# Kernel tuning notes

Hardware: AMD Instinct MI355X
Metric: run time of the kernel (lower is better)

Reference implementation:

```python
import jax, jax.numpy as jnp
import numpy as np

B, T, C, H = 1, 2048, 1024, 16
K = C // H


def _ln(x, g, b):
    m = x.mean(-1, keepdims=True)
    v = ((x - m) ** 2).mean(-1, keepdims=True)
    return (x - m) * jax.lax.rsqrt(v + 1e-5) * g + b


def setup_inputs() -> dict:
    key = jax.random.key(0)
    ks = jax.random.split(key, 16)
    n = lambda k, s, sc=1.0: jax.random.normal(k, s, jnp.float32) * sc
    u = lambda k, s: jax.random.uniform(k, s, jnp.float32)
    ws = C ** -0.5
    return {
        "x": n(ks[0], (B, T, C)),
        "shift_state": n(ks[1], (B, C)),
        "time_maa_x": u(ks[2], (1, 1, C)),
        "time_maa_r": u(ks[3], (1, 1, C)),
        "time_maa_k": u(ks[4], (1, 1, C)),
        "time_maa_v": u(ks[5], (1, 1, C)),
        "time_maa_w1": n(ks[6], (C, 96), 0.01),
        "time_maa_w2": n(ks[7], (3, 32, C), 0.01),
        "headavg_w1": n(ks[8], (C, 4 * 2 * H), 0.01),
        "headavg_w2": n(ks[9], (4, 2 * H, H), 0.01),
        "w_r": n(ks[10], (C, C), ws),
        "w_k": n(ks[11], (C, C), ws),
        "w_v": n(ks[12], (C, C), ws),
        "w_o": n(ks[13], (C, C), ws),
        "ln_r_g": jnp.ones((C,)), "ln_r_b": jnp.zeros((C,)),
        "ln_k_g": jnp.ones((C,)), "ln_k_b": jnp.zeros((C,)),
        "ln_v_g": jnp.ones((C,)), "ln_v_b": jnp.zeros((C,)),
        "ln_x_g": jnp.ones((C,)), "ln_x_b": jnp.zeros((C,)),
    }


def reference(x, shift_state, time_maa_x, time_maa_r, time_maa_k, time_maa_v,
              time_maa_w1, time_maa_w2, headavg_w1, headavg_w2,
              w_r, w_k, w_v, w_o,
              ln_r_g, ln_r_b, ln_k_g, ln_k_b, ln_v_g, ln_v_b, ln_x_g, ln_x_b):
    Bs, Ts, Cs = x.shape
    Hh = headavg_w2.shape[-1]
    Kk = Cs // Hh

    # token shift
    dxprev = jnp.concatenate([shift_state[:, None, :], x[:, :-1]], axis=1) - x

    # LoRA token-shift mixing
    xxx = jnp.tanh((x + dxprev * time_maa_x) @ time_maa_w1)       # [B,T,3*32]
    mix = jnp.einsum('btnd,ndc->nbtc', xxx.reshape(Bs, Ts, 3, -1), time_maa_w2)
    mq, mk, mv = mix[0], mix[1], mix[2]
    xq = x + dxprev * (time_maa_r + mq)
    xk = x + dxprev * (time_maa_k + mk)
    xv = x + dxprev * (time_maa_v + mv)

    q = _ln(xq @ w_r, ln_r_g, ln_r_b).reshape(Bs, Ts, Hh, Kk).transpose(0, 2, 1, 3)
    k = _ln(xk @ w_k, ln_k_g, ln_k_b).reshape(Bs, Ts, Hh, Kk).transpose(0, 2, 1, 3)
    v = _ln(xv @ w_v, ln_v_g, ln_v_b).reshape(Bs, Ts, Hh, Kk).transpose(0, 2, 1, 3)

    # per-head LoRA score mixing coefficients
    ha = jnp.tanh(x @ headavg_w1).reshape(Bs, Ts, 4, -1)          # [B,T,4,2H]
    hm = jnp.einsum('btnd,ndh->nbth', ha, headavg_w2) / Hh        # [4,B,T,H]
    pre_q, pre_k, post_q, post_k = hm[0], hm[1], hm[2], hm[3]

    scale = Kk ** -0.5
    y = jnp.einsum('bhtk,bhsk->bhts', q * scale, k)               # [B,H,T,S]
    y = y + jnp.einsum('bhts,bth->bts', y, pre_q)[:, None]
    y = y + jnp.einsum('bhts,bsh->bts', y, pre_k)[:, None]

    # causal ALiBi bias
    rel = (jnp.arange(Ts)[:, None] - jnp.arange(Ts)[None, :]).astype(x.dtype)
    slopes = (2.0 ** (-8.0 * jnp.arange(1, Hh + 1, dtype=x.dtype) / Hh))
    bias = jnp.where(rel >= 0, -slopes[:, None, None] * rel, jnp.asarray(-1e9, x.dtype))
    y = y + bias[None]

    y = jax.nn.softmax(y, axis=-1)
    y = y + jnp.einsum('bhts,bth->bts', y, post_q)[:, None]
    y = y + jnp.einsum('bhts,bsh->bts', y, post_k)[:, None]

    out = jnp.einsum('bhts,bhsv->bhtv', y, v).transpose(0, 2, 1, 3).reshape(Bs, Ts, Cs)
    out = _ln(out, ln_x_g, ln_x_b) @ w_o
    return out
```

## Files before the change

### kernel.cpp

```cpp
#include <hip/hip_runtime.h>
#include <cstdint>
#include <cstddef>


#define C_DIM 1024
#define HEADS 16
#define TQ 16
#define SCH 256
#define PADS 40
#define EPS 36

typedef unsigned short ushort_t;
typedef __attribute__((ext_vector_type(8))) short bf16x8;
typedef __attribute__((ext_vector_type(4))) float f32x4;

#define MFMA16(a, b, c) __builtin_amdgcn_mfma_f32_16x16x32_bf16(a, b, c, 0, 0, 0)

__device__ __forceinline__ unsigned int f2bf_u(float f) {
  unsigned int u = __float_as_uint(f);
  return (u + 0x7fffu + ((u >> 16) & 1u)) >> 16;
}
__device__ __forceinline__ float bf2f(ushort_t u) {
  return __uint_as_float(((unsigned int)u) << 16);
}
__device__ __forceinline__ void pack4(ushort_t* dst, float x0, float x1,
                                      float x2, float x3) {
  uint2 v;
  v.x = f2bf_u(x0) | (f2bf_u(x1) << 16);
  v.y = f2bf_u(x2) | (f2bf_u(x3) << 16);
  *(uint2*)dst = v;
}
__device__ __forceinline__ void mlmerge(float& M, float& L, float m2, float l2) {
  float nm = fmaxf(M, m2);
  float ea = (M  <= -1e29f) ? 0.f : __expf(M - nm);
  float eb = (m2 <= -1e29f) ? 0.f : __expf(m2 - nm);
  L = L * ea + l2 * eb;
  M = nm;
}

__global__ __launch_bounds__(256) void prep_kernel(
    const float* __restrict__ x, const float* __restrict__ shift,
    const float* __restrict__ maa_x,
    float* __restrict__ dxprev, ushort_t* __restrict__ zbf,
    ushort_t* __restrict__ xbf)
{
  const int t = blockIdx.x;
  const int c = threadIdx.x * 4;
  const size_t base = (size_t)t * C_DIM + c;
  const float4 xc = *(const float4*)&x[base];
  const float4 xp = (t == 0) ? *(const float4*)&shift[c]
                             : *(const float4*)&x[base - C_DIM];
  const float4 mx = *(const float4*)&maa_x[c];
  float4 d;
  d.x = xp.x - xc.x; d.y = xp.y - xc.y; d.z = xp.z - xc.z; d.w = xp.w - xc.w;
  *(float4*)&dxprev[base] = d;
  pack4(&zbf[base], xc.x + d.x*mx.x, xc.y + d.y*mx.y,
        xc.z + d.z*mx.z, xc.w + d.w*mx.w);
  pack4(&xbf[base], xc.x, xc.y, xc.z, xc.w);
}

__global__ __launch_bounds__(256) void wlora_prep(
    const float* __restrict__ w1, const float* __restrict__ hw1,
    ushort_t* __restrict__ wlt)
{
  __shared__ float tile[32][33];
  const int k0 = blockIdx.x*32, j0 = blockIdx.y*32;
  const int r = threadIdx.x >> 3, c4 = (threadIdx.x & 7) * 4;
  const float* W = (j0 < 96) ? w1 : hw1;
  const int stride = (j0 < 96) ? 96 : 128;
  const int jo = (j0 < 96) ? j0 : j0 - 96;
  const float4 v = *(const float4*)&W[(size_t)(k0+r)*stride + jo + c4];
  tile[r][c4+0] = v.x; tile[r][c4+1] = v.y;
  tile[r][c4+2] = v.z; tile[r][c4+3] = v.w;
  __syncthreads();
  pack4(&wlt[(size_t)(j0+r)*C_DIM + k0 + c4],
        tile[c4+0][r], tile[c4+1][r], tile[c4+2][r], tile[c4+3][r]);
}

__global__ __launch_bounds__(64) void lora_gemm(
    const ushort_t* __restrict__ zbf, const ushort_t* __restrict__ xbf,
    const ushort_t* __restrict__ wlt, float* __restrict__ xxx,
    float* __restrict__ ha)
{
  const int nt = blockIdx.y;
  const int bm = blockIdx.x * 32;
  const ushort_t* A = (nt < 3) ? zbf : xbf;
  const int wrow = nt * 32;
  const int lane = threadIdx.x;
  const int l15 = lane & 15, g = lane >> 4;
  f32x4 acc[2][2];
  #pragma unroll
  for (int i = 0; i < 2; i++)
    #pragma unroll
    for (int j = 0; j < 2; j++) acc[i][j] = (f32x4){0.f,0.f,0.f,0.f};
  bf16x8 a0[2], b0[2], a1[2], b1[2];
  #define LLA(dst, kk) { \
    dst[0] = *(const bf16x8*)&A[(size_t)(bm + l15)*C_DIM + (kk) + g*8]; \
    dst[1] = *(const bf16x8*)&A[(size_t)(bm + 16 + l15)*C_DIM + (kk) + g*8]; }
  #define LLB(dst, kk) { \
    dst[0] = *(const bf16x8*)&wlt[(size_t)(wrow + l15)*C_DIM + (kk) + g*8]; \
    dst[1] = *(const bf16x8*)&wlt[(size_t)(wrow + 16 + l15)*C_DIM + (kk) + g*8]; }
  LLA(a0, 0); LLB(b0, 0);
  for (int k0 = 0; k0 < C_DIM; k0 += 64) {
    LLA(a1, k0+32); LLB(b1, k0+32);
    #pragma unroll
    for (int i = 0; i < 2; i++)
      #pragma unroll
      for (int j = 0; j < 2; j++) acc[i][j] = MFMA16(a0[i], b0[j], acc[i][j]);
    if (k0 + 64 < C_DIM) { LLA(a0, k0+64); LLB(b0, k0+64); }
    #pragma unroll
    for (int i = 0; i < 2; i++)
      #pragma unroll
      for (int j = 0; j < 2; j++) acc[i][j] = MFMA16(a1[i], b1[j], acc[i][j]);
  }
  #undef LLA
  #undef LLB
  #pragma unroll
  for (int i = 0; i < 2; i++)
    #pragma unroll
    for (int j = 0; j < 2; j++)
      #pragma unroll
      for (int r = 0; r < 4; r++) {
        const int t = bm + i*16 + g*4 + r;
        const int col = wrow + j*16 + l15;
        const float val = tanhf(acc[i][j][r]);
        if (nt < 3) xxx[(size_t)t*96 + col] = val;
        else        ha[(size_t)t*128 + col - 96] = val;
      }
}

__global__ __launch_bounds__(256) void mix_kernel(
    const float* __restrict__ x, const float* __restrict__ dxp,
    const float* __restrict__ xxx,
    const float* __restrict__ maa_r, const float* __restrict__ maa_k,
    const float* __restrict__ maa_v, const float* __restrict__ w2,
    ushort_t* __restrict__ xq, ushort_t* __restrict__ xk,
    ushort_t* __restrict__ xv)
{
  __shared__ float xs[8][96];
  const int t0 = blockIdx.x * 8;
  const int tid = threadIdx.x;
  #pragma unroll
  for (int i = 0; i < 3; i++) {
    const int u = tid + i*256;
    if (u < 768) {
      const int r = u / 96, cc = u % 96;
      xs[r][cc] = xxx[(size_t)(t0+r)*96 + cc];
    }
  }
  __syncthreads();
  const int c = tid * 4;
  float4 xc[8], dx[8];
  #pragma unroll
  for (int r = 0; r < 8; r++) {
    xc[r] = *(const float4*)&x[(size_t)(t0+r)*C_DIM + c];
    dx[r] = *(const float4*)&dxp[(size_t)(t0+r)*C_DIM + c];
  }
  const float* maas[3] = {maa_r, maa_k, maa_v};
  ushort_t* outs[3] = {xq, xk, xv};
  #pragma unroll
  for (int n = 0; n < 3; n++) {
    const float4 mv = *(const float4*)&maas[n][c];
    float m[8][4];
    #pragma unroll
    for (int r = 0; r < 8; r++) {
      m[r][0] = mv.x; m[r][1] = mv.y; m[r][2] = mv.z; m[r][3] = mv.w;
    }
    #pragma unroll 8
    for (int d = 0; d < 32; d++) {
      const float4 w = *(const float4*)&w2[((size_t)n*32 + d)*C_DIM + c];
      #pragma unroll
      for (int r = 0; r < 8; r++) {
        const float xv2 = xs[r][n*32 + d];
        m[r][0] += xv2*w.x; m[r][1] += xv2*w.y;
        m[r][2] += xv2*w.z; m[r][3] += xv2*w.w;
      }
    }
    #pragma unroll
    for (int r = 0; r < 8; r++)
      pack4(&outs[n][(size_t)(t0+r)*C_DIM + c],
            xc[r].x + dx[r].x*m[r][0], xc[r].y + dx[r].y*m[r][1],
            xc[r].z + dx[r].z*m[r][2], xc[r].w + dx[r].w*m[r][3]);
  }
}

__global__ __launch_bounds__(256) void hm_kernel(
    const float* __restrict__ ha, const float* __restrict__ hw2,
    float* __restrict__ hm, int T)
{
  const int t = blockIdx.x*4 + (threadIdx.x >> 6);
  const int u = threadIdx.x & 63;
  const int n = u >> 4, h = u & 15;
  float s = 0.f;
  #pragma unroll 8
  for (int d = 0; d < 32; d++)
    s += ha[(size_t)t*128 + n*32 + d] * hw2[(size_t)(n*32 + d)*16 + h];
  hm[((size_t)n*T + t)*16 + h] = s * (1.f/16.f);
}

__global__ __launch_bounds__(256) void wprep_kernel(
    const float* __restrict__ w0, const float* __restrict__ w1,
    const float* __restrict__ w2, const float* __restrict__ w3,
    ushort_t* __restrict__ o0, ushort_t* __restrict__ o1,
    ushort_t* __restrict__ o2, ushort_t* __restrict__ o3)
{
  const float* W; ushort_t* O;
  if (blockIdx.z == 0)      { W = w0; O = o0; }
  else if (blockIdx.z == 1) { W = w1; O = o1; }
  else if (blockIdx.z == 2) { W = w2; O = o2; }
  else                      { W = w3; O = o3; }
  __shared__ float tile[32][33];
  const int k0 = blockIdx.x*32, n0 = blockIdx.y*32;
  const int r = threadIdx.x >> 3, c4 = (threadIdx.x & 7) * 4;
  const float4 v = *(const float4*)&W[(size_t)(k0+r)*C_DIM + n0 + c4];
  tile[r][c4+0] = v.x; tile[r][c4+1] = v.y;
  tile[r][c4+2] = v.z; tile[r][c4+3] = v.w;
  __syncthreads();
  pack4(&O[(size_t)(n0+r)*C_DIM + k0 + c4],
        tile[c4+0][r], tile[c4+1][r], tile[c4+2][r], tile[c4+3][r]);
}

__global__ __launch_bounds__(64) void gemm_bf16(
    const ushort_t* __restrict__ A, const ushort_t* __restrict__ Bt,
    float* __restrict__ Cm)
{
  const int bid = blockIdx.x;
  const int bn = (bid & 15) * 64;
  const int bm = (bid >> 4) * 32;
  const int lane = threadIdx.x;
  const int l15 = lane & 15, g = lane >> 4;
  f32x4 acc[2][4];
  #pragma unroll
  for (int i = 0; i < 2; i++)
    #pragma unroll
    for (int j = 0; j < 4; j++) acc[i][j] = (f32x4){0.f,0.f,0.f,0.f};
  bf16x8 a0[2], b0[4], a1[2], b1[4];
  #define LGA(dst, kk) { \
    _Pragma("unroll") \
    for (int i = 0; i < 2; i++) \
      dst[i] = *(const bf16x8*)&A[(size_t)(bm + i*16 + l15)*C_DIM + (kk) + g*8]; }
  #define LGB(dst, kk) { \
    _Pragma("unroll") \
    for (int j = 0; j < 4; j++) \
      dst[j] = *(const bf16x8*)&Bt[(size_t)(bn + j*16 + l15)*C_DIM + (kk) + g*8]; }
  LGA(a0, 0); LGB(b0, 0);
  for (int k0 = 0; k0 < C_DIM; k0 += 64) {
    LGA(a1, k0+32); LGB(b1, k0+32);
    #pragma unroll
    for (int i = 0; i < 2; i++)
      #pragma unroll
      for (int j = 0; j < 4; j++) acc[i][j] = MFMA16(a0[i], b0[j], acc[i][j]);
    if (k0 + 64 < C_DIM) { LGA(a0, k0+64); LGB(b0, k0+64); }
    #pragma unroll
    for (int i = 0; i < 2; i++)
      #pragma unroll
      for (int j = 0; j < 4; j++) acc[i][j] = MFMA16(a1[i], b1[j], acc[i][j]);
  }
  #undef LGA
  #undef LGB
  #pragma unroll
  for (int i = 0; i < 2; i++)
    #pragma unroll
    for (int j = 0; j < 4; j++)
      #pragma unroll
      for (int r = 0; r < 4; r++)
        Cm[(size_t)(bm + i*16 + g*4 + r)*C_DIM + bn + j*16 + l15] = acc[i][j][r];
}

__global__ __launch_bounds__(256) void ln_rows(
    const float* __restrict__ in, ushort_t* __restrict__ outp,
    const float* __restrict__ g, const float* __restrict__ b, float scale)
{
  __shared__ float red[4];
  const int t = blockIdx.x;
  const int tid = threadIdx.x;
  const int c = tid*4;
  const float4 v = *(const float4*)&in[(size_t)t*C_DIM + c];
  float s = v.x+v.y+v.z+v.w;
  #pragma unroll
  for (int off = 32; off > 0; off >>= 1) s += __shfl_down(s, off, 64);
  if ((tid & 63) == 0) red[tid >> 6] = s;
  __syncthreads();
  const float mean = (red[0]+red[1]+red[2]+red[3]) * (1.0f/C_DIM);
  __syncthreads();
  const float d0 = v.x-mean, d1 = v.y-mean, d2 = v.z-mean, d3 = v.w-mean;
  float q = d0*d0 + d1*d1 + d2*d2 + d3*d3;
  #pragma unroll
  for (int off = 32; off > 0; off >>= 1) q += __shfl_down(q, off, 64);
  if ((tid & 63) == 0) red[tid >> 6] = q;
  __syncthreads();
  const float var = (red[0]+red[1]+red[2]+red[3]) * (1.0f/C_DIM);
  const float rstd = rsqrtf(var + 1e-5f);
  const float4 gv = *(const float4*)&g[c];
  const float4 bv = *(const float4*)&b[c];
  pack4(outp + (size_t)t*C_DIM + c,
        (d0*rstd*gv.x + bv.x)*scale, (d1*rstd*gv.y + bv.y)*scale,
        (d2*rstd*gv.z + bv.z)*scale, (d3*rstd*gv.w + bv.w)*scale);
}

__global__ __launch_bounds__(256) void vtrans_kernel(
    const ushort_t* __restrict__ vbf, ushort_t* __restrict__ Vt, int T)
{
  __shared__ ushort_t tile[32][36];
  const int t0 = blockIdx.x*32, c0 = blockIdx.y*32;
  const int r = threadIdx.x >> 3, c4 = (threadIdx.x & 7) * 4;
  const uint2 raw = *(const uint2*)&vbf[(size_t)(t0+r)*C_DIM + c0 + c4];
  tile[r][c4+0] = (ushort_t)(raw.x & 0xffffu);
  tile[r][c4+1] = (ushort_t)(raw.x >> 16);
  tile[r][c4+2] = (ushort_t)(raw.y & 0xffffu);
  tile[r][c4+3] = (ushort_t)(raw.y >> 16);
  __syncthreads();
  uint2 w;
  w.x = (unsigned)tile[c4+0][r] | ((unsigned)tile[c4+1][r] << 16);
  w.y = (unsigned)tile[c4+2][r] | ((unsigned)tile[c4+3][r] << 16);
  *(uint2*)&Vt[(size_t)(c0+r)*T + t0 + c4] = w;
}

__global__ __launch_bounds__(256) void qek_prep(
    const ushort_t* __restrict__ qbf, const ushort_t* __restrict__ kbf,
    const float* __restrict__ hmb, ushort_t* __restrict__ Qe,
    ushort_t* __restrict__ Ke, float* __restrict__ spo_g, int T)
{
  const int t = blockIdx.x;
  const int tid = threadIdx.x;
  const int c4 = tid * 4;
  const int h = tid >> 4;
  float sp = 0.f, so = 0.f;
  #pragma unroll
  for (int q4 = 0; q4 < 4; q4++) {
    const float4 v = *(const float4*)&hmb[((size_t)1*T + t)*16 + q4*4];
    sp += v.x + v.y + v.z + v.w;
    const float4 o = *(const float4*)&hmb[((size_t)3*T + t)*16 + q4*4];
    so += o.x + o.y + o.z + o.w;
  }
  if (tid == 0) spo_g[t] = so;
  const float preq = hmb[((size_t)0*T + t)*16 + h];
  const float prek = hmb[((size_t)1*T + t)*16 + h];
  const uint2 qr = *(const uint2*)&qbf[(size_t)t*C_DIM + c4];
  const uint2 kr = *(const uint2*)&kbf[(size_t)t*C_DIM + c4];
  float qv[4], kv[4];
  qv[0] = bf2f((ushort_t)(qr.x & 0xffffu)); qv[1] = bf2f((ushort_t)(qr.x >> 16));
  qv[2] = bf2f((ushort_t)(qr.y & 0xffffu)); qv[3] = bf2f((ushort_t)(qr.y >> 16));
  kv[0] = bf2f((ushort_t)(kr.x & 0xffffu)); kv[1] = bf2f((ushort_t)(kr.x >> 16));
  kv[2] = bf2f((ushort_t)(kr.y & 0xffffu)); kv[3] = bf2f((ushort_t)(kr.y >> 16));
  const size_t rb = (size_t)t * 2048;
  pack4(&Qe[rb + c4], qv[0]*preq, qv[1]*preq, qv[2]*preq, qv[3]*preq);
  *(uint2*)&Qe[rb + 1024 + c4] = qr;
  const float osp = 1.f + sp;
  pack4(&Ke[rb + c4], kv[0]*osp, kv[1]*osp, kv[2]*osp, kv[3]*osp);
  pack4(&Ke[rb + 1024 + c4], kv[0]*prek, kv[1]*prek, kv[2]*prek, kv[3]*prek);
}

__global__ __launch_bounds__(64) void e_gemm(
    const ushort_t* __restrict__ Qe, const ushort_t* __restrict__ Ke,
    float* __restrict__ E, int T)
{
  const int bm = blockIdx.y * 32;
  const int bn = blockIdx.x * 64;
  if (bn > bm + 31) return;
  const int lane = threadIdx.x;
  const int l15 = lane & 15, g = lane >> 4;
  const int KD = 2048;
  f32x4 acc[2][4];
  #pragma unroll
  for (int i = 0; i < 2; i++)
    #pragma unroll
    for (int j = 0; j < 4; j++) acc[i][j] = (f32x4){0.f,0.f,0.f,0.f};
  bf16x8 a0[2], b0[4], a1[2], b1[4];
  #define LEA(dst, kk) { \
    _Pragma("unroll") \
    for (int i = 0; i < 2; i++) \
      dst[i] = *(const bf16x8*)&Qe[(size_t)(bm + i*16 + l15)*KD + (kk) + g*8]; }
  #define LEB(dst, kk) { \
    _Pragma("unroll") \
    for (int j = 0; j < 4; j++) \
      dst[j] = *(const bf16x8*)&Ke[(size_t)(bn + j*16 + l15)*KD + (kk) + g*8]; }
  LEA(a0, 0); LEB(b0, 0);
  for (int k0 = 0; k0 < KD; k0 += 64) {
    LEA(a1, k0+32); LEB(b1, k0+32);
    #pragma unroll
    for (int i = 0; i < 2; i++)
      #pragma unroll
      for (int j = 0; j < 4; j++) acc[i][j] = MFMA16(a0[i], b0[j], acc[i][j]);
    if (k0 + 64 < KD) { LEA(a0, k0+64); LEB(b0, k0+64); }
    #pragma unroll
    for (int i = 0; i < 2; i++)
      #pragma unroll
      for (int j = 0; j < 4; j++) acc[i][j] = MFMA16(a1[i], b1[j], acc[i][j]);
  }
  #undef LEA
  #undef LEB
  #pragma unroll
  for (int i = 0; i < 2; i++)
    #pragma unroll
    for (int j = 0; j < 4; j++)
      #pragma unroll
      for (int r = 0; r < 4; r++)
        E[(size_t)(bm + i*16 + g*4 + r)*T + bn + j*16 + l15] = acc[i][j][r];
}

__global__ __launch_bounds__(512) void attn_stats(
    const ushort_t* __restrict__ qbf, const ushort_t* __restrict__ kbf,
    const float* __restrict__ E, float* __restrict__ part_m,
    float* __restrict__ part_l, int T)
{
  const int tbi = (int)blockIdx.y;
  const int tb = (T/TQ) - 1 - tbi;
  const int sc = (tbi & 1) ? (7 - (int)blockIdx.x) : (int)blockIdx.x;
  const int t0 = tb * TQ;
  const int sbeg = sc * SCH;
  if (sbeg >= t0 + TQ) return;
  const int send = (sbeg + SCH < t0 + TQ) ? (sbeg + SCH) : (t0 + TQ);

  const int tid = threadIdx.x;
  const int w = tid >> 6, lane = tid & 63, l15 = lane & 15, g = lane >> 4;
  const int hh[2] = {w, w + 8};
  bf16x8 qf[2][2];
  float slope[2];
  #pragma unroll
  for (int hd = 0; hd < 2; hd++) {
    #pragma unroll
    for (int kc = 0; kc < 2; kc++)
      qf[hd][kc] = *(const bf16x8*)
          &qbf[(size_t)(t0 + l15)*C_DIM + hh[hd]*64 + kc*32 + g*8];
    slope[hd] = exp2f(-0.5f * (float)(hh[hd] + 1));
  }
  float mrun[2] = {-1e30f, -1e30f}, lrun[2] = {0.f, 0.f};

  bf16x8 kf[2][2][2];
  float4 ef[2];
  #define LOADK(sbase) { \
    _Pragma("unroll") \
    for (int hd = 0; hd < 2; hd++) \
      _Pragma("unroll") \
      for (int sh = 0; sh < 2; sh++) \
        _Pragma("unroll") \
        for (int kc = 0; kc < 2; kc++) \
          kf[hd][sh][kc] = *(const bf16x8*)&kbf[ \
              (size_t)((sbase) + sh*16 + l15)*C_DIM + hh[hd]*64 + kc*32 + g*8]; }
  #define LOADE(sbase) { \
    _Pragma("unroll") \
    for (int sh = 0; sh < 2; sh++) \
      ef[sh] = *(const float4*)&E[(size_t)(t0 + l15)*T + (sbase) + sh*16 + g*4]; }
  LOADK(sbeg); LOADE(sbeg);

  for (int s1 = sbeg; s1 < send; s1 += 32) {
    f32x4 acc[2][2];
    #pragma unroll
    for (int hd = 0; hd < 2; hd++)
      #pragma unroll
      for (int sh = 0; sh < 2; sh++) acc[hd][sh] = (f32x4){0.f,0.f,0.f,0.f};
    #pragma unroll
    for (int hd = 0; hd < 2; hd++)
      #pragma unroll
      for (int sh = 0; sh < 2; sh++)
        #pragma unroll
        for (int kc = 0; kc < 2; kc++)
          acc[hd][sh] = MFMA16(kf[hd][sh][kc], qf[hd][kc], acc[hd][sh]);
    float efc[2][4];
    #pragma unroll
    for (int sh = 0; sh < 2; sh++) *(float4*)efc[sh] = ef[sh];
    {
      const int snx = (s1 + 32 < send) ? s1 + 32 : s1;
      LOADK(snx); LOADE(snx);
    }
    #pragma unroll
    for (int hd = 0; hd < 2; hd++) {
      const int t = t0 + l15;
      #pragma unroll
      for (int sh = 0; sh < 2; sh++)
        #pragma unroll
        for (int r = 0; r < 4; r++) {
          const int s = s1 + sh*16 + g*4 + r;
          if (s <= t) {
            const float y3 = acc[hd][sh][r] + efc[sh][r]
                - slope[hd]*(float)(t - s);
            const float d = y3 - mrun[hd];
            if (d > 0.f) { lrun[hd] = lrun[hd]*__expf(-d) + 1.f; mrun[hd] = y3; }
            else lrun[hd] += __expf(d);
          }
        }
    }
  }
  #undef LOADK
  #undef LOADE
  #pragma unroll
  for (int hd = 0; hd < 2; hd++) {
    float M = mrun[hd], L = lrun[hd];
    #pragma unroll
    for (int mask = 16; mask < 64; mask <<= 1) {
      const float M2 = __shfl_xor(M, mask, 64);
      const float L2 = __shfl_xor(L, mask, 64);
      mlmerge(M, L, M2, L2);
    }
    if (g == 0) {
      part_m[(size_t)(sc*HEADS + hh[hd])*T + t0 + l15] = M;
      part_l[(size_t)(sc*HEADS + hh[hd])*T + t0 + l15] = L;
    }
  }
}

__global__ __launch_bounds__(256) void ml_combine(
    const float* __restrict__ part_m, const float* __restrict__ part_l,
    float* __restrict__ m_fin, float* __restrict__ linv, int T)
{
  const int idx = blockIdx.x*256 + threadIdx.x;
  const int t = idx & (T - 1);
  const int nsc = (t >> 8) + 1;
  float M = -1e30f, L = 0.f;
  for (int sc = 0; sc < nsc; sc++)
    mlmerge(M, L, part_m[(size_t)sc*HEADS*T + idx],
            part_l[(size_t)sc*HEADS*T + idx]);
  m_fin[idx] = M;
  linv[idx] = 1.f / L;
}

__global__ __launch_bounds__(512) void attn_apply(
    const ushort_t* __restrict__ qbf, const ushort_t* __restrict__ kbf,
    const ushort_t* __restrict__ Vt, const float* __restrict__ E,
    const float* __restrict__ hmb, const float* __restrict__ spo_g,
    const float* __restrict__ m_fin, const float* __restrict__ linv,
    float* __restrict__ P, int T)
{
  __shared__ ushort_t ybuf[HEADS*TQ*PADS];
  __shared__ float ep[TQ*EPS];

  const int tbi = (int)blockIdx.y;
  const int tb = (T/TQ) - 1 - tbi;
  const int sc = (tbi & 1) ? (7 - (int)blockIdx.x) : (int)blockIdx.x;
  const int t0 = tb * TQ;
  const int sbeg = sc * SCH;
  if (sbeg >= t0 + TQ) return;
  const int send = (sbeg + SCH < t0 + TQ) ? (sbeg + SCH) : (t0 + TQ);
  const int prow0 = T*sc - 128*sc*(sc-1) - SCH*sc;

  const int tid = threadIdx.x;
  const int w = tid >> 6, lane = tid & 63, l15 = lane & 15, g = lane >> 4;

  const int hh[2] = {w, w + 8};
  bf16x8 qf[2][2];
  float mt[2], li[2], slope[2];
  #pragma unroll
  for (int hd = 0; hd < 2; hd++) {
    #pragma unroll
    for (int kc = 0; kc < 2; kc++)
      qf[hd][kc] = *(const bf16x8*)
          &qbf[(size_t)(t0 + l15)*C_DIM + hh[hd]*64 + kc*32 + g*8];
    mt[hd] = m_fin[(size_t)hh[hd]*T + t0 + l15];
    li[hd] = linv[(size_t)hh[hd]*T + t0 + l15];
    slope[hd] = exp2f(-0.5f * (float)(hh[hd] + 1));
  }
  f32x4 oacc[2][4];
  #pragma unroll
  for (int hd = 0; hd < 2; hd++)
    #pragma unroll
    for (int vf = 0; vf < 4; vf++) oacc[hd][vf] = (f32x4){0.f,0.f,0.f,0.f};

  for (int s1 = sbeg; s1 < send; s1 += 32) {
    f32x4 acc[2][2];
    #pragma unroll
    for (int hd = 0; hd < 2; hd++)
      #pragma unroll
      for (int sh = 0; sh < 2; sh++) acc[hd][sh] = (f32x4){0.f,0.f,0.f,0.f};
    float4 ef[2];
    #pragma unroll
    for (int sh = 0; sh < 2; sh++)
      ef[sh] = *(const float4*)&E[(size_t)(t0 + l15)*T + s1 + sh*16 + g*4];
    #pragma unroll
    for (int hd = 0; hd < 2; hd++)
      #pragma unroll
      for (int sh = 0; sh < 2; sh++)
        #pragma unroll
        for (int kc = 0; kc < 2; kc++) {
          const bf16x8 kf = *(const bf16x8*)
              &kbf[(size_t)(s1 + sh*16 + l15)*C_DIM + hh[hd]*64 + kc*32 + g*8];
          acc[hd][sh] = MFMA16(kf, qf[hd][kc], acc[hd][sh]);
        }
    #pragma unroll
    for (int hd = 0; hd < 2; hd++) {
      const int t = t0 + l15;
      #pragma unroll
      for (int sh = 0; sh < 2; sh++) {
        #pragma unroll
        for (int r = 0; r < 4; r++) {
          const int s = s1 + sh*16 + g*4 + r;
          float p = 0.f;
          if (s <= t) {
            const float y3 = acc[hd][sh][r] + ef[sh][r]
                - slope[hd]*(float)(t - s);
            p = __expf(y3 - mt[hd]) * li[hd];
          }
          acc[hd][sh][r] = p;
        }
        pack4(&ybuf[(size_t)(hh[hd]*TQ + l15)*PADS + sh*16 + g*4],
              acc[hd][sh][0], acc[hd][sh][1], acc[hd][sh][2], acc[hd][sh][3]);
      }
    }
    __syncthreads();
    if (tid < 128) {
      const int tcq = tid >> 3, sq = tid & 7;
      const int s0g = s1 + sq*4;
      const float* hoqr = &hmb[((size_t)2*T + t0 + tcq)*16];
      float a4[4] = {0.f,0.f,0.f,0.f}, b4[4] = {0.f,0.f,0.f,0.f};
      #pragma unroll
      for (int hq4 = 0; hq4 < 4; hq4++) {
        float hqa[4];
        *(float4*)hqa = *(const float4*)&hoqr[hq4*4];
        float hka[4][4];
        #pragma unroll
        for (int c = 0; c < 4; c++)
          *(float4*)hka[c] =
              *(const float4*)&hmb[((size_t)3*T + s0g + c)*16 + hq4*4];
        #pragma unroll
        for (int j = 0; j < 4; j++) {
          const uint2 yr = *(const uint2*)
              &ybuf[((hq4*4 + j)*TQ + tcq)*PADS + sq*4];
          float yv[4];
          yv[0] = bf2f((ushort_t)(yr.x & 0xffffu));
          yv[1] = bf2f((ushort_t)(yr.x >> 16));
          yv[2] = bf2f((ushort_t)(yr.y & 0xffffu));
          yv[3] = bf2f((ushort_t)(yr.y >> 16));
          #pragma unroll
          for (int c = 0; c < 4; c++) {
            a4[c] += yv[c] * hqa[j];
            b4[c] += yv[c] * hka[c][j];
          }
        }
      }
      float ssum[4];
      *(float4*)ssum = *(const float4*)&spo_g[s0g];
      float4 eo;
      eo.x = a4[0]*(1.f + ssum[0]) + b4[0];
      eo.y = a4[1]*(1.f + ssum[1]) + b4[1];
      eo.z = a4[2]*(1.f + ssum[2]) + b4[2];
      eo.w = a4[3]*(1.f + ssum[3]) + b4[3];
      *(float4*)&ep[tcq*EPS + sq*4] = eo;
    }
    __syncthreads();
    bf16x8 vv[2][4];
    #pragma unroll
    for (int hd = 0; hd < 2; hd++)
      #pragma unroll
      for (int vf = 0; vf < 4; vf++)
        vv[hd][vf] = *(const bf16x8*)
            &Vt[(size_t)(hh[hd]*64 + vf*16 + l15)*T + s1 + g*8];
    {
      float epv[2][4];
      #pragma unroll
      for (int sh = 0; sh < 2; sh++)
        *(float4*)epv[sh] = *(const float4*)&ep[l15*EPS + sh*16 + g*4];
      #pragma unroll
      for (int hd = 0; hd < 2; hd++)
        #pragma unroll
        for (int sh = 0; sh < 2; sh++)
          pack4(&ybuf[(size_t)(hh[hd]*TQ + l15)*PADS + sh*16 + g*4],
                acc[hd][sh][0] + epv[sh][0], acc[hd][sh][1] + epv[sh][1],
                acc[hd][sh][2] + epv[sh][2], acc[hd][sh][3] + epv[sh][3]);
    }
    #pragma unroll
    for (int hd = 0; hd < 2; hd++) {
      const bf16x8 pa = *(const bf16x8*)
          &ybuf[(size_t)(hh[hd]*TQ + l15)*PADS + g*8];
      #pragma unroll
      for (int vf = 0; vf < 4; vf++)
        oacc[hd][vf] = MFMA16(pa, vv[hd][vf], oacc[hd][vf]);
    }
  }
  #pragma unroll
  for (int hd = 0; hd < 2; hd++)
    #pragma unroll
    for (int vf = 0; vf < 4; vf++)
      #pragma unroll
      for (int r = 0; r < 4; r++)
        P[(size_t)(prow0 + t0 + g*4 + r)*C_DIM + hh[hd]*64 + vf*16 + l15]
            = oacc[hd][vf][r];
}

__global__ __launch_bounds__(256) void reduce_ln(
    const float* __restrict__ P, ushort_t* __restrict__ outp,
    const float* __restrict__ g, const float* __restrict__ b, int T)
{
  __shared__ float red[4];
  const int t = blockIdx.x;
  const int tid = threadIdx.x;
  const int c = tid*4;
  const int nsc = (t >> 8) + 1;
  float4 v = make_float4(0.f, 0.f, 0.f, 0.f);
  int off = 0;
  for (int sc = 0; sc < nsc; sc++) {
    const int row = off + t - sc*SCH;
    const float4 pv = *(const float4*)&P[(size_t)row*C_DIM + c];
    v.x += pv.x; v.y += pv.y; v.z += pv.z; v.w += pv.w;
    off += T - SCH*sc;
  }
  float s = v.x+v.y+v.z+v.w;
  #pragma unroll
  for (int o = 32; o > 0; o >>= 1) s += __shfl_down(s, o, 64);
  if ((tid & 63) == 0) red[tid >> 6] = s;
  __syncthreads();
  const float mean = (red[0]+red[1]+red[2]+red[3]) * (1.0f/C_DIM);
  __syncthreads();
  const float d0 = v.x-mean, d1 = v.y-mean, d2 = v.z-mean, d3 = v.w-mean;
  float q = d0*d0 + d1*d1 + d2*d2 + d3*d3;
  #pragma unroll
  for (int o = 32; o > 0; o >>= 1) q += __shfl_down(q, o, 64);
  if ((tid & 63) == 0) red[tid >> 6] = q;
  __syncthreads();
  const float var = (red[0]+red[1]+red[2]+red[3]) * (1.0f/C_DIM);
  const float rstd = rsqrtf(var + 1e-5f);
  const float4 gv = *(const float4*)&g[c];
  const float4 bv = *(const float4*)&b[c];
  pack4(outp + (size_t)t*C_DIM + c,
        d0*rstd*gv.x + bv.x, d1*rstd*gv.y + bv.y,
        d2*rstd*gv.z + bv.z, d3*rstd*gv.w + bv.w);
}

extern "C" void kernel_launch(void* const* d_in, const int* in_sizes, int n_in,
                              void* d_out, int out_size, void* d_ws, size_t ws_size,
                              hipStream_t stream)
{
  const float* x      = (const float*)d_in[0];
  const float* shift  = (const float*)d_in[1];
  const float* maa_x  = (const float*)d_in[2];
  const float* maa_r  = (const float*)d_in[3];
  const float* maa_k  = (const float*)d_in[4];
  const float* maa_v  = (const float*)d_in[5];
  const float* w1     = (const float*)d_in[6];
  const float* w2     = (const float*)d_in[7];
  const float* hw1    = (const float*)d_in[8];
  const float* hw2    = (const float*)d_in[9];
  const float* w_r    = (const float*)d_in[10];
  const float* w_k    = (const float*)d_in[11];
  const float* w_v    = (const float*)d_in[12];
  const float* w_o    = (const float*)d_in[13];
  const float* ln_r_g = (const float*)d_in[14];
  const float* ln_r_b = (const float*)d_in[15];
  const float* ln_k_g = (const float*)d_in[16];
  const float* ln_k_b = (const float*)d_in[17];
  const float* ln_v_g = (const float*)d_in[18];
  const float* ln_v_b = (const float*)d_in[19];
  const float* ln_x_g = (const float*)d_in[20];
  const float* ln_x_b = (const float*)d_in[21];

  const int T = in_sizes[0] / C_DIM;
  const size_t MM = (size_t)T * C_DIM;
  const size_t HF = MM / 2;

  float* ws = (float*)d_ws;
  float*    P      = ws;
  float*    dxprev = ws;
  ushort_t* zbf    = (ushort_t*)(ws + MM);
  ushort_t* xbf    = (ushort_t*)(ws + MM + HF);
  float*    gtmp   = ws + 2*MM;
  ushort_t* xqb    = (ushort_t*)(ws + 3*MM);
  ushort_t* xkb    = (ushort_t*)(ws + 3*MM + HF);
  ushort_t* xvb    = (ushort_t*)(ws + 4*MM);
  ushort_t* Qe = (ushort_t*)gtmp;
  ushort_t* Ke = (ushort_t*)(ws + 3*MM);
  float* base2 = ws + 4*MM + HF;
  ushort_t* qbf = (ushort_t*)(base2 + 0*HF);
  ushort_t* kbf = (ushort_t*)(base2 + 1*HF);
  ushort_t* vbf = (ushort_t*)(base2 + 2*HF);
  ushort_t* Vt  = (ushort_t*)(base2 + 3*HF);
  ushort_t* wtr = (ushort_t*)(base2 + 4*HF);
  ushort_t* wtk = wtr + (size_t)C_DIM*C_DIM;
  ushort_t* wtv = wtk + (size_t)C_DIM*C_DIM;
  ushort_t* wto = wtv + (size_t)C_DIM*C_DIM;
  float* after_w = base2 + 4*HF + (size_t)2*C_DIM*C_DIM;
  ushort_t* wlt = (ushort_t*)after_w;
  float* xxx    = after_w + 131072;
  float* ha     = xxx + (size_t)T*96;
  float* hmb    = ha + (size_t)T*128;
  float* part_m = hmb + (size_t)4*T*16;
  float* part_l = part_m + (size_t)8*HEADS*T;
  float* m_fin  = part_l + (size_t)8*HEADS*T;
  float* linv   = m_fin + (size_t)HEADS*T;
  float* spo_g  = linv + (size_t)HEADS*T;
  float* abf_f  = spo_g + (size_t)T;
  ushort_t* abf = (ushort_t*)abf_f;
  float* Ebuf   = abf_f + HF;

  prep_kernel<<<T, 256, 0, stream>>>(x, shift, maa_x, dxprev, zbf, xbf);
  wlora_prep<<<dim3(C_DIM/32, 7), 256, 0, stream>>>(w1, hw1, wlt);
  lora_gemm<<<dim3(T/32, 7), 64, 0, stream>>>(zbf, xbf, wlt, xxx, ha);
  mix_kernel<<<T/8, 256, 0, stream>>>(x, dxprev, xxx, maa_r, maa_k, maa_v, w2,
                                      xqb, xkb, xvb);
  hm_kernel<<<T/4, 256, 0, stream>>>(ha, hw2, hmb, T);
  wprep_kernel<<<dim3(32, 32, 4), 256, 0, stream>>>(
      w_r, w_k, w_v, w_o, wtr, wtk, wtv, wto);

  const int ggemm = (T/32) * (C_DIM/64);
  gemm_bf16<<<ggemm, 64, 0, stream>>>(xqb, wtr, gtmp);
  ln_rows<<<T, 256, 0, stream>>>(gtmp, qbf, ln_r_g, ln_r_b, 0.125f);
  gemm_bf16<<<ggemm, 64, 0, stream>>>(xkb, wtk, gtmp);
  ln_rows<<<T, 256, 0, stream>>>(gtmp, kbf, ln_k_g, ln_k_b, 1.0f);
  gemm_bf16<<<ggemm, 64, 0, stream>>>(xvb, wtv, gtmp);
  ln_rows<<<T, 256, 0, stream>>>(gtmp, vbf, ln_v_g, ln_v_b, 1.0f);
  vtrans_kernel<<<dim3(T/32, C_DIM/32), 256, 0, stream>>>(vbf, Vt, T);

  qek_prep<<<T, 256, 0, stream>>>(qbf, kbf, hmb, Qe, Ke, spo_g, T);
  e_gemm<<<dim3(T/64, T/32), 64, 0, stream>>>(Qe, Ke, Ebuf, T);

  attn_stats<<<dim3(8, T/TQ), 512, 0, stream>>>(
      qbf, kbf, Ebuf, part_m, part_l, T);
  ml_combine<<<(HEADS*T)/256, 256, 0, stream>>>(part_m, part_l, m_fin, linv, T);
  attn_apply<<<dim3(8, T/TQ), 512, 0, stream>>>(
      qbf, kbf, Vt, Ebuf, hmb, spo_g, m_fin, linv, P, T);

  reduce_ln<<<T, 256, 0, stream>>>(P, abf, ln_x_g, ln_x_b, T);
  gemm_bf16<<<ggemm, 64, 0, stream>>>(abf, wto, (float*)d_out);
}
```

Measured before the change: 576.9 us.

## Cache pre-softmax scores in fp16 between attention passes and shrink GEMM tiles

attn_stats now writes the computed pre-softmax score (QK plus E term plus ALiBi) to a compact fp16 buffer indexed by a triangular offset. attn_apply reads those scores back instead of reloading q/k and redoing the QK MFMAs and E reads. Separately, the projection GEMMs and e_gemm move from 32x64 to 32x32 tiles, which doubles the number of blocks and gives finer causal skipping in e_gemm. The costs are extra global traffic for the score buffer, fp16 rounding of the scores, and less operand reuse per block in the GEMMs.

```diff
diff --git a/kernel.cpp b/kernel.cpp
--- a/kernel.cpp
+++ b/kernel.cpp
@@ -1,4 +1,5 @@
 #include <hip/hip_runtime.h>
+#include <hip/hip_fp16.h>
 #include <cstdint>
 #include <cstddef>
 
@@ -36,6 +37,11 @@
   float eb = (m2 <= -1e29f) ? 0.f : __expf(m2 - nm);
   L = L * ea + l2 * eb;
   M = nm;
+}
+__device__ __forceinline__ int y3_off(int tbi) {
+  const int m = tbi >> 1;
+  const int S = m*(m-1) + ((tbi & 1) ? m : 0);
+  return 64*tbi - S;
 }
 
 __global__ __launch_bounds__(256) void prep_kernel(
@@ -225,23 +231,23 @@
     float* __restrict__ Cm)
 {
   const int bid = blockIdx.x;
-  const int bn = (bid & 15) * 64;
-  const int bm = (bid >> 4) * 32;
+  const int bn = (bid & 31) * 32;
+  const int bm = (bid >> 5) * 32;
   const int lane = threadIdx.x;
   const int l15 = lane & 15, g = lane >> 4;
-  f32x4 acc[2][4];
+  f32x4 acc[2][2];
   #pragma unroll
   for (int i = 0; i < 2; i++)
     #pragma unroll
-    for (int j = 0; j < 4; j++) acc[i][j] = (f32x4){0.f,0.f,0.f,0.f};
-  bf16x8 a0[2], b0[4], a1[2], b1[4];
+    for (int j = 0; j < 2; j++) acc[i][j] = (f32x4){0.f,0.f,0.f,0.f};
+  bf16x8 a0[2], b0[2], a1[2], b1[2];
   #define LGA(dst, kk) { \
     _Pragma("unroll") \
     for (int i = 0; i < 2; i++) \
       dst[i] = *(const bf16x8*)&A[(size_t)(bm + i*16 + l15)*C_DIM + (kk) + g*8]; }
   #define LGB(dst, kk) { \
     _Pragma("unroll") \
-    for (int j = 0; j < 4; j++) \
+    for (int j = 0; j < 2; j++) \
       dst[j] = *(const bf16x8*)&Bt[(size_t)(bn + j*16 + l15)*C_DIM + (kk) + g*8]; }
   LGA(a0, 0); LGB(b0, 0);
   for (int k0 = 0; k0 < C_DIM; k0 += 64) {
@@ -249,19 +255,19 @@
     #pragma unroll
     for (int i = 0; i < 2; i++)
       #pragma unroll
-      for (int j = 0; j < 4; j++) acc[i][j] = MFMA16(a0[i], b0[j], acc[i][j]);
+      for (int j = 0; j < 2; j++) acc[i][j] = MFMA16(a0[i], b0[j], acc[i][j]);
     if (k0 + 64 < C_DIM) { LGA(a0, k0+64); LGB(b0, k0+64); }
     #pragma unroll
     for (int i = 0; i < 2; i++)
       #pragma unroll
-      for (int j = 0; j < 4; j++) acc[i][j] = MFMA16(a1[i], b1[j], acc[i][j]);
+      for (int j = 0; j < 2; j++) acc[i][j] = MFMA16(a1[i], b1[j], acc[i][j]);
   }
   #undef LGA
   #undef LGB
   #pragma unroll
   for (int i = 0; i < 2; i++)
     #pragma unroll
-    for (int j = 0; j < 4; j++)
+    for (int j = 0; j < 2; j++)
       #pragma unroll
       for (int r = 0; r < 4; r++)
         Cm[(size_t)(bm + i*16 + g*4 + r)*C_DIM + bn + j*16 + l15] = acc[i][j][r];
@@ -355,25 +361,25 @@
     const ushort_t* __restrict__ Qe, const ushort_t* __restrict__ Ke,
     float* __restrict__ E, int T)
 {
+  if ((int)blockIdx.x > (int)blockIdx.y) return;
   const int bm = blockIdx.y * 32;
-  const int bn = blockIdx.x * 64;
-  if (bn > bm + 31) return;
+  const int bn = blockIdx.x * 32;
   const int lane = threadIdx.x;
   const int l15 = lane & 15, g = lane >> 4;
   const int KD = 2048;
-  f32x4 acc[2][4];
+  f32x4 acc[2][2];
   #pragma unroll
   for (int i = 0; i < 2; i++)
     #pragma unroll
-    for (int j = 0; j < 4; j++) acc[i][j] = (f32x4){0.f,0.f,0.f,0.f};
-  bf16x8 a0[2], b0[4], a1[2], b1[4];
+    for (int j = 0; j < 2; j++) acc[i][j] = (f32x4){0.f,0.f,0.f,0.f};
+  bf16x8 a0[2], b0[2], a1[2], b1[2];
   #define LEA(dst, kk) { \
     _Pragma("unroll") \
     for (int i = 0; i < 2; i++) \
       dst[i] = *(const bf16x8*)&Qe[(size_t)(bm + i*16 + l15)*KD + (kk) + g*8]; }
   #define LEB(dst, kk) { \
     _Pragma("unroll") \
-    for (int j = 0; j < 4; j++) \
+    for (int j = 0; j < 2; j++) \
       dst[j] = *(const bf16x8*)&Ke[(size_t)(bn + j*16 + l15)*KD + (kk) + g*8]; }
   LEA(a0, 0); LEB(b0, 0);
   for (int k0 = 0; k0 < KD; k0 += 64) {
@@ -381,19 +387,19 @@
     #pragma unroll
     for (int i = 0; i < 2; i++)
       #pragma unroll
-      for (int j = 0; j < 4; j++) acc[i][j] = MFMA16(a0[i], b0[j], acc[i][j]);
+      for (int j = 0; j < 2; j++) acc[i][j] = MFMA16(a0[i], b0[j], acc[i][j]);
     if (k0 + 64 < KD) { LEA(a0, k0+64); LEB(b0, k0+64); }
     #pragma unroll
     for (int i = 0; i < 2; i++)
       #pragma unroll
-      for (int j = 0; j < 4; j++) acc[i][j] = MFMA16(a1[i], b1[j], acc[i][j]);
+      for (int j = 0; j < 2; j++) acc[i][j] = MFMA16(a1[i], b1[j], acc[i][j]);
   }
   #undef LEA
   #undef LEB
   #pragma unroll
   for (int i = 0; i < 2; i++)
     #pragma unroll
-    for (int j = 0; j < 4; j++)
+    for (int j = 0; j < 2; j++)
       #pragma unroll
       for (int r = 0; r < 4; r++)
         E[(size_t)(bm + i*16 + g*4 + r)*T + bn + j*16 + l15] = acc[i][j][r];
@@ -402,7 +408,7 @@
 __global__ __launch_bounds__(512) void attn_stats(
     const ushort_t* __restrict__ qbf, const ushort_t* __restrict__ kbf,
     const float* __restrict__ E, float* __restrict__ part_m,
-    float* __restrict__ part_l, int T)
+    float* __restrict__ part_l, ushort_t* __restrict__ y3d, int T)
 {
   const int tbi = (int)blockIdx.y;
   const int tb = (T/TQ) - 1 - tbi;
@@ -411,6 +417,7 @@
   const int sbeg = sc * SCH;
   if (sbeg >= t0 + TQ) return;
   const int send = (sbeg + SCH < t0 + TQ) ? (sbeg + SCH) : (t0 + TQ);
+  const int offT = y3_off(tbi);
 
   const int tid = threadIdx.x;
   const int w = tid >> 6, lane = tid & 63, l15 = lane & 15, g = lane >> 4;
@@ -464,22 +471,30 @@
       const int snx = (s1 + 32 < send) ? s1 + 32 : s1;
       LOADK(snx); LOADE(snx);
     }
+    ushort_t* slot = y3d + ((size_t)(offT + (s1 >> 5))*512 + tid)*16;
     #pragma unroll
     for (int hd = 0; hd < 2; hd++) {
       const int t = t0 + l15;
       #pragma unroll
-      for (int sh = 0; sh < 2; sh++)
+      for (int sh = 0; sh < 2; sh++) {
+        float y3v[4];
         #pragma unroll
         for (int r = 0; r < 4; r++) {
           const int s = s1 + sh*16 + g*4 + r;
+          y3v[r] = acc[hd][sh][r] + efc[sh][r] - slope[hd]*(float)(t - s);
           if (s <= t) {
-            const float y3 = acc[hd][sh][r] + efc[sh][r]
-                - slope[hd]*(float)(t - s);
-            const float d = y3 - mrun[hd];
-            if (d > 0.f) { lrun[hd] = lrun[hd]*__expf(-d) + 1.f; mrun[hd] = y3; }
+            const float d = y3v[r] - mrun[hd];
+            if (d > 0.f) { lrun[hd] = lrun[hd]*__expf(-d) + 1.f; mrun[hd] = y3v[r]; }
             else lrun[hd] += __expf(d);
           }
         }
+        __half2 h0 = __floats2half2_rn(y3v[0], y3v[1]);
+        __half2 h1 = __floats2half2_rn(y3v[2], y3v[3]);
+        uint2 pk;
+        pk.x = *(unsigned*)&h0;
+        pk.y = *(unsigned*)&h1;
+        *(uint2*)(slot + (hd*2 + sh)*4) = pk;
+      }
     }
   }
   #undef LOADK
@@ -516,8 +531,7 @@
 }
 
 __global__ __launch_bounds__(512) void attn_apply(
-    const ushort_t* __restrict__ qbf, const ushort_t* __restrict__ kbf,
-    const ushort_t* __restrict__ Vt, const float* __restrict__ E,
+    const ushort_t* __restrict__ y3d, const ushort_t* __restrict__ Vt,
     const float* __restrict__ hmb, const float* __restrict__ spo_g,
     const float* __restrict__ m_fin, const float* __restrict__ linv,
     float* __restrict__ P, int T)
@@ -533,22 +547,16 @@
   if (sbeg >= t0 + TQ) return;
   const int send = (sbeg + SCH < t0 + TQ) ? (sbeg + SCH) : (t0 + TQ);
   const int prow0 = T*sc - 128*sc*(sc-1) - SCH*sc;
+  const int offT = y3_off(tbi);
 
   const int tid = threadIdx.x;
   const int w = tid >> 6, lane = tid & 63, l15 = lane & 15, g = lane >> 4;
-
   const int hh[2] = {w, w + 8};
-  bf16x8 qf[2][2];
-  float mt[2], li[2], slope[2];
+  float mt[2], li[2];
   #pragma unroll
   for (int hd = 0; hd < 2; hd++) {
-    #pragma unroll
-    for (int kc = 0; kc < 2; kc++)
-      qf[hd][kc] = *(const bf16x8*)
-          &qbf[(size_t)(t0 + l15)*C_DIM + hh[hd]*64 + kc*32 + g*8];
     mt[hd] = m_fin[(size_t)hh[hd]*T + t0 + l15];
     li[hd] = linv[(size_t)hh[hd]*T + t0 + l15];
-    slope[hd] = exp2f(-0.5f * (float)(hh[hd] + 1));
   }
   f32x4 oacc[2][4];
   #pragma unroll
@@ -557,39 +565,22 @@
     for (int vf = 0; vf < 4; vf++) oacc[hd][vf] = (f32x4){0.f,0.f,0.f,0.f};
 
   for (int s1 = sbeg; s1 < send; s1 += 32) {
+    const ushort_t* slot = y3d + ((size_t)(offT + (s1 >> 5))*512 + tid)*16;
     f32x4 acc[2][2];
-    #pragma unroll
-    for (int hd = 0; hd < 2; hd++)
-      #pragma unroll
-      for (int sh = 0; sh < 2; sh++) acc[hd][sh] = (f32x4){0.f,0.f,0.f,0.f};
-    float4 ef[2];
-    #pragma unroll
-    for (int sh = 0; sh < 2; sh++)
-      ef[sh] = *(const float4*)&E[(size_t)(t0 + l15)*T + s1 + sh*16 + g*4];
-    #pragma unroll
-    for (int hd = 0; hd < 2; hd++)
-      #pragma unroll
-      for (int sh = 0; sh < 2; sh++)
-        #pragma unroll
-        for (int kc = 0; kc < 2; kc++) {
-          const bf16x8 kf = *(const bf16x8*)
-              &kbf[(size_t)(s1 + sh*16 + l15)*C_DIM + hh[hd]*64 + kc*32 + g*8];
-          acc[hd][sh] = MFMA16(kf, qf[hd][kc], acc[hd][sh]);
-        }
     #pragma unroll
     for (int hd = 0; hd < 2; hd++) {
       const int t = t0 + l15;
       #pragma unroll
       for (int sh = 0; sh < 2; sh++) {
+        const uint2 pk = *(const uint2*)(slot + (hd*2 + sh)*4);
+        const float2 f0 = __half22float2(*(const __half2*)&pk.x);
+        const float2 f1 = __half22float2(*(const __half2*)&pk.y);
+        const float y3v[4] = {f0.x, f0.y, f1.x, f1.y};
         #pragma unroll
         for (int r = 0; r < 4; r++) {
           const int s = s1 + sh*16 + g*4 + r;
           float p = 0.f;
-          if (s <= t) {
-            const float y3 = acc[hd][sh][r] + ef[sh][r]
-                - slope[hd]*(float)(t - s);
-            p = __expf(y3 - mt[hd]) * li[hd];
-          }
+          if (s <= t) p = __expf(y3v[r] - mt[hd]) * li[hd];
           acc[hd][sh][r] = p;
         }
         pack4(&ybuf[(size_t)(hh[hd]*TQ + l15)*PADS + sh*16 + g*4],
@@ -779,6 +770,7 @@
   float* abf_f  = spo_g + (size_t)T;
   ushort_t* abf = (ushort_t*)abf_f;
   float* Ebuf   = abf_f + HF;
+  ushort_t* y3d = (ushort_t*)(Ebuf + (size_t)T*T);
 
   prep_kernel<<<T, 256, 0, stream>>>(x, shift, maa_x, dxprev, zbf, xbf);
   wlora_prep<<<dim3(C_DIM/32, 7), 256, 0, stream>>>(w1, hw1, wlt);
@@ -789,7 +781,7 @@
   wprep_kernel<<<dim3(32, 32, 4), 256, 0, stream>>>(
       w_r, w_k, w_v, w_o, wtr, wtk, wtv, wto);
 
-  const int ggemm = (T/32) * (C_DIM/64);
+  const int ggemm = (T/32) * (C_DIM/32);
   gemm_bf16<<<ggemm, 64, 0, stream>>>(xqb, wtr, gtmp);
   ln_rows<<<T, 256, 0, stream>>>(gtmp, qbf, ln_r_g, ln_r_b, 0.125f);
   gemm_bf16<<<ggemm, 64, 0, stream>>>(xkb, wtk, gtmp);
@@ -799,13 +791,13 @@
   vtrans_kernel<<<dim3(T/32, C_DIM/32), 256, 0, stream>>>(vbf, Vt, T);
 
   qek_prep<<<T, 256, 0, stream>>>(qbf, kbf, hmb, Qe, Ke, spo_g, T);
-  e_gemm<<<dim3(T/64, T/32), 64, 0, stream>>>(Qe, Ke, Ebuf, T);
+  e_gemm<<<dim3(T/32, T/32), 64, 0, stream>>>(Qe, Ke, Ebuf, T);
 
   attn_stats<<<dim3(8, T/TQ), 512, 0, stream>>>(
-      qbf, kbf, Ebuf, part_m, part_l, T);
+      qbf, kbf, Ebuf, part_m, part_l, y3d, T);
   ml_combine<<<(HEADS*T)/256, 256, 0, stream>>>(part_m, part_l, m_fin, linv, T);
   attn_apply<<<dim3(8, T/TQ), 512, 0, stream>>>(
-      qbf, kbf, Vt, Ebuf, hmb, spo_g, m_fin, linv, P, T);
+      y3d, Vt, hmb, spo_g, m_fin, linv, P, T);
 
   reduce_ln<<<T, 256, 0, stream>>>(P, abf, ln_x_g, ln_x_b, T);
   gemm_bf16<<<ggemm, 64, 0, stream>>>(abf, wto, (float*)d_out);
```

After: 579.1 us. Within noise of the previous version (+0.4%).
